# Kernel optimization log

Hardware: AMD Instinct MI355X
Metric: run time of the kernel (lower is better)

The kernel has to match this reference:

```python
import jax, jax.numpy as jnp
import numpy as np

NUM_EXPERTS = 16
TOP_K = 2
HIDDEN = 2048
INTER = 1408
TOKENS = 4096


def setup_inputs() -> dict:
    key = jax.random.key(0)
    k0, k1, k2, k3, k4 = jax.random.split(key, 5)
    scale = 0.02
    return {
        "hidden_states": jax.random.normal(k0, (TOKENS, HIDDEN), jnp.float32),
        "router_logits": jax.random.normal(k1, (TOKENS, NUM_EXPERTS), jnp.float32),
        # SwiGLU expert weights, stacked over the expert dim.
        "w_gate": jax.random.normal(k2, (NUM_EXPERTS, HIDDEN, INTER), jnp.float32) * scale,
        "w_up": jax.random.normal(k3, (NUM_EXPERTS, HIDDEN, INTER), jnp.float32) * scale,
        "w_down": jax.random.normal(k4, (NUM_EXPERTS, INTER, HIDDEN), jnp.float32) * scale,
    }


def reference(hidden_states, router_logits, w_gate, w_up, w_down):
    # Routing (router_use_softmax=False branch): topk on raw logits,
    # then softmax over the selected top-k logits.
    topk_weights, topk_ids = jax.lax.top_k(router_logits, TOP_K)  # [T,K]
    topk_weights = jax.nn.softmax(topk_weights, axis=-1)

    T = hidden_states.shape[0]
    # Dense combine matrix [T, E]: weight of expert e for token t (0 if not selected).
    combine = jnp.zeros((T, NUM_EXPERTS), hidden_states.dtype)
    combine = combine.at[jnp.arange(T)[:, None], topk_ids].add(topk_weights)

    # Expert SwiGLU FFNs, computed densely over all tokens per expert and
    # masked/weighted by the combine matrix (same math as gather->FFN->scatter).
    g = jnp.einsum("th,ehi->eti", hidden_states, w_gate)  # [E,T,I]
    u = jnp.einsum("th,ehi->eti", hidden_states, w_up)    # [E,T,I]
    a = jax.nn.silu(g) * u                                  # [E,T,I]
    y = jnp.einsum("eti,eih->eth", a, w_down)             # [E,T,H]

    # Weighted scatter-combine: sum_e combine[t,e] * y[e,t,:]
    return jnp.einsum("eth,te->th", y, combine)            # [T,H]
```

## Files before the change

### kernel.cpp

```cpp
#include <hip/hip_runtime.h>
#include <hip/hip_bf16.h>
#include <cstdint>

#define NTOK 4096
#define NEXP 16
#define HID 2048
#define INTER 1408
#define BK 32
#define LDA 40
#define MAXTILES 80
#define GU_NB 22
#define DN_NB 32
#define GU_GRID (GU_NB * MAXTILES)
#define DN_GRID (DN_NB * MAXTILES)

typedef __attribute__((ext_vector_type(8))) short bf16x8;
typedef __attribute__((ext_vector_type(4))) float f32x4;


__device__ inline unsigned pack_bf16(float lo, float hi) {
  unsigned a = __builtin_bit_cast(unsigned, lo) + 0x8000u;
  unsigned b = __builtin_bit_cast(unsigned, hi) + 0x8000u;
  return __builtin_amdgcn_perm(b, a, 0x07060302u);
}

__global__ void k_router(const float* __restrict__ logits, int* __restrict__ topk_id,
                         float* __restrict__ topk_w, int* __restrict__ counts) {
  int t = blockIdx.x * blockDim.x + threadIdx.x;
  if (t >= NTOK) return;
  const float* l = logits + (size_t)t * NEXP;
  float b0 = -1e30f, b1 = -1e30f; int i0 = 0, i1 = 0;
#pragma unroll
  for (int i = 0; i < NEXP; i++) {
    float v = l[i];
    if (v > b0) { b1 = b0; i1 = i0; b0 = v; i0 = i; }
    else if (v > b1) { b1 = v; i1 = i; }
  }
  float e = __expf(b1 - b0);
  float inv = 1.f / (1.f + e);
  topk_id[t * 2] = i0; topk_id[t * 2 + 1] = i1;
  topk_w[t * 2] = inv; topk_w[t * 2 + 1] = e * inv;
  atomicAdd(&counts[i0], 1);
  atomicAdd(&counts[i1], 1);
}

__global__ void k_build(int* __restrict__ ws_i) {
  if (threadIdx.x == 0) {
    int off = 0, nt = 0;
    for (int e = 0; e < NEXP; e++) {
      int c = ws_i[e];
      ws_i[32 + e] = off;
      int tiles = (c + 127) >> 7;
      for (int mt = 0; mt < tiles; mt++) { ws_i[64 + nt] = e; ws_i[144 + nt] = mt; nt++; }
      off += c;
    }
    ws_i[48] = nt;
  }
}

__global__ void k_scatter(const int* __restrict__ topk_id, const float* __restrict__ topk_w,
                          int* __restrict__ ws_i, int* __restrict__ list_tok,
                          float* __restrict__ list_w, int* __restrict__ slot_of) {
  int t = blockIdx.x * blockDim.x + threadIdx.x;
  if (t >= NTOK) return;
#pragma unroll
  for (int k = 0; k < 2; k++) {
    int e = topk_id[t * 2 + k];
    int slot = ws_i[32 + e] + atomicAdd(&ws_i[16 + e], 1);
    list_tok[slot] = t;
    list_w[slot] = topk_w[t * 2 + k];
    slot_of[t * 2 + k] = slot;
  }
}

__global__ __launch_bounds__(256) void k_gather(const float* __restrict__ hidden,
                                                const int* __restrict__ list_tok,
                                                unsigned short* __restrict__ Ab) {
  int s = blockIdx.x, tx = threadIdx.x;
  int t = list_tok[s];
  const float4* src = (const float4*)(hidden + (size_t)t * HID) + tx * 2;
  float4 a = src[0], b = src[1];
  uint4 w = make_uint4(pack_bf16(a.x, a.y), pack_bf16(a.z, a.w),
                       pack_bf16(b.x, b.y), pack_bf16(b.z, b.w));
  ((uint4*)(Ab + (size_t)s * HID))[tx] = w;
}

__global__ __launch_bounds__(256, 4) void k_gateup(
    const unsigned short* __restrict__ Ab, const float* __restrict__ w_gate,
    const float* __restrict__ w_up, const int* __restrict__ ws_i,
    __hip_bfloat16* __restrict__ act) {
  __shared__ unsigned short sA[128 * LDA];
  __shared__ unsigned short sBg[64 * LDA];
  __shared__ unsigned short sBu[64 * LDA];

  int bid = blockIdx.x;
  int w = (bid & 7) * (GU_GRID / 8) + (bid >> 3);
  int tileId = w / GU_NB;
  int n0 = (w - tileId * GU_NB) * 64;
  if (tileId >= ws_i[48]) return;
  int e = ws_i[64 + tileId];
  int mt = ws_i[144 + tileId];
  int c = ws_i[e];
  int offE = ws_i[32 + e];
  int m0 = mt * 128;
  int tid = threadIdx.x;

  int lane = tid & 63;
  int wave = tid >> 6;
  int wm = wave & 1, wn = wave >> 1;

  int ar = tid >> 1;
  int ah = (tid & 1) * 16;
  int rA = m0 + ar; int rrA = rA < c ? rA : c - 1;
  const unsigned short* aSrc = Ab + (size_t)(offE + rrA) * HID + ah;

  int bn = tid & 63;
  int bkg = tid >> 6;
  const float* bgSrc = w_gate + (size_t)e * HID * INTER + n0 + bn + (size_t)(bkg * 8) * INTER;
  const float* buSrc = w_up   + (size_t)e * HID * INTER + n0 + bn + (size_t)(bkg * 8) * INTER;

  f32x4 accG[4][2], accU[4][2];
#pragma unroll
  for (int i = 0; i < 4; i++)
#pragma unroll
    for (int j = 0; j < 2; j++) { accG[i][j] = (f32x4)(0.f); accU[i][j] = (f32x4)(0.f); }

  int kq = (lane >> 4) * 8;
  int ml = lane & 15;

  uint4 a0r, a1r; float g[8], u[8];
  {
    const uint4* ap = (const uint4*)aSrc;
    a0r = ap[0]; a1r = ap[1];
#pragma unroll
    for (int j = 0; j < 8; j++) { g[j] = bgSrc[(size_t)j * INTER]; u[j] = buSrc[(size_t)j * INTER]; }
  }

  for (int k0 = 0; k0 < HID; k0 += BK) {
    __syncthreads();
    *(uint4*)&sA[ar * LDA + ah] = a0r;
    *(uint4*)&sA[ar * LDA + ah + 8] = a1r;
    *(uint4*)&sBg[bn * LDA + bkg * 8] = make_uint4(
        pack_bf16(g[0], g[1]), pack_bf16(g[2], g[3]),
        pack_bf16(g[4], g[5]), pack_bf16(g[6], g[7]));
    *(uint4*)&sBu[bn * LDA + bkg * 8] = make_uint4(
        pack_bf16(u[0], u[1]), pack_bf16(u[2], u[3]),
        pack_bf16(u[4], u[5]), pack_bf16(u[6], u[7]));
    __syncthreads();

    if (k0 + BK < HID) {
      const uint4* ap = (const uint4*)(aSrc + k0 + BK);
      a0r = ap[0]; a1r = ap[1];
      const float* bg = bgSrc + (size_t)(k0 + BK) * INTER;
      const float* bu = buSrc + (size_t)(k0 + BK) * INTER;
#pragma unroll
      for (int j = 0; j < 8; j++) { g[j] = bg[(size_t)j * INTER]; u[j] = bu[(size_t)j * INTER]; }
    }

    bf16x8 af[4], bgf[2], buf2[2];
#pragma unroll
    for (int ni = 0; ni < 2; ni++) {
      bgf[ni] = *(const bf16x8*)&sBg[(wn * 32 + ni * 16 + ml) * LDA + kq];
      buf2[ni] = *(const bf16x8*)&sBu[(wn * 32 + ni * 16 + ml) * LDA + kq];
    }
#pragma unroll
    for (int mi = 0; mi < 4; mi++)
      af[mi] = *(const bf16x8*)&sA[(wm * 64 + mi * 16 + ml) * LDA + kq];
#pragma unroll
    for (int mi = 0; mi < 4; mi++)
#pragma unroll
      for (int ni = 0; ni < 2; ni++) {
        accG[mi][ni] = __builtin_amdgcn_mfma_f32_16x16x32_bf16(af[mi], bgf[ni], accG[mi][ni], 0, 0, 0);
        accU[mi][ni] = __builtin_amdgcn_mfma_f32_16x16x32_bf16(af[mi], buf2[ni], accU[mi][ni], 0, 0, 0);
      }
  }

  int rq = (lane >> 4) * 4;
#pragma unroll
  for (int mi = 0; mi < 4; mi++)
#pragma unroll
    for (int r = 0; r < 4; r++) {
      int mrow = wm * 64 + mi * 16 + rq + r;
      int mglob = m0 + mrow;
      if (mglob < c) {
        size_t arow = (size_t)(offE + mglob);
#pragma unroll
        for (int ni = 0; ni < 2; ni++) {
          float gv = accG[mi][ni][r], uv = accU[mi][ni][r];
          float av = gv / (1.f + __expf(-gv)) * uv;
          int ncol = n0 + wn * 32 + ni * 16 + ml;
          act[arow * INTER + ncol] = __float2bfloat16(av);
        }
      }
    }
}

__global__ __launch_bounds__(256, 4) void k_down(
    const __hip_bfloat16* __restrict__ act, const float* __restrict__ w_down,
    const int* __restrict__ ws_i, const float* __restrict__ list_w,
    unsigned short* __restrict__ y) {
  __shared__ unsigned short sA[128 * LDA];
  __shared__ unsigned short sB[64 * LDA];
  __shared__ float sW[128];

  int bid = blockIdx.x;
  int w = (bid & 7) * (DN_GRID / 8) + (bid >> 3);
  int tileId = w >> 5;
  int n0 = (w & 31) * 64;
  if (tileId >= ws_i[48]) return;
  int e = ws_i[64 + tileId];
  int mt = ws_i[144 + tileId];
  int c = ws_i[e];
  int offE = ws_i[32 + e];
  int m0 = mt * 128;
  int tid = threadIdx.x;

  if (tid < 128) {
    int r = m0 + tid;
    int rr = r < c ? r : c - 1;
    sW[tid] = list_w[offE + rr];
  }

  int lane = tid & 63;
  int wave = tid >> 6;
  int wm = wave & 1, wn = wave >> 1;
  f32x4 acc[4][2];
#pragma unroll
  for (int i = 0; i < 4; i++)
#pragma unroll
    for (int j = 0; j < 2; j++) acc[i][j] = (f32x4)(0.f);

  int ar = tid >> 1;
  int ah = (tid & 1) * 16;
  int rA = m0 + ar; int rrA = rA < c ? rA : c - 1;
  const unsigned short* aSrc = (const unsigned short*)act + (size_t)(offE + rrA) * INTER + ah;

  int bn = tid & 63;
  int bkg = tid >> 6;
  const float* bSrc = w_down + (size_t)e * INTER * HID + (size_t)(bkg * 8) * HID + n0 + bn;

  int kq = (lane >> 4) * 8;
  int ml = lane & 15;

  uint4 a0r, a1r; float b[8];
  {
    const uint4* ap = (const uint4*)aSrc;
    a0r = ap[0]; a1r = ap[1];
#pragma unroll
    for (int j = 0; j < 8; j++) b[j] = bSrc[(size_t)j * HID];
  }

  for (int k0 = 0; k0 < INTER; k0 += BK) {
    __syncthreads();
    *(uint4*)&sA[ar * LDA + ah] = a0r;
    *(uint4*)&sA[ar * LDA + ah + 8] = a1r;
    *(uint4*)&sB[bn * LDA + bkg * 8] = make_uint4(
        pack_bf16(b[0], b[1]), pack_bf16(b[2], b[3]),
        pack_bf16(b[4], b[5]), pack_bf16(b[6], b[7]));
    __syncthreads();

    if (k0 + BK < INTER) {
      const uint4* ap = (const uint4*)(aSrc + k0 + BK);
      a0r = ap[0]; a1r = ap[1];
      const float* bp = bSrc + (size_t)(k0 + BK) * HID;
#pragma unroll
      for (int j = 0; j < 8; j++) b[j] = bp[(size_t)j * HID];
    }

    bf16x8 af[4], bf[2];
#pragma unroll
    for (int ni = 0; ni < 2; ni++)
      bf[ni] = *(const bf16x8*)&sB[(wn * 32 + ni * 16 + ml) * LDA + kq];
#pragma unroll
    for (int mi = 0; mi < 4; mi++)
      af[mi] = *(const bf16x8*)&sA[(wm * 64 + mi * 16 + ml) * LDA + kq];
#pragma unroll
    for (int mi = 0; mi < 4; mi++)
#pragma unroll
      for (int ni = 0; ni < 2; ni++)
        acc[mi][ni] = __builtin_amdgcn_mfma_f32_16x16x32_bf16(af[mi], bf[ni], acc[mi][ni], 0, 0, 0);
  }

  int rq = (lane >> 4) * 4;
#pragma unroll
  for (int mi = 0; mi < 4; mi++)
#pragma unroll
    for (int r = 0; r < 4; r++) {
      int mrow = wm * 64 + mi * 16 + rq + r;
      if (m0 + mrow < c) {
        float w2 = sW[mrow];
        size_t yrow = (size_t)(offE + m0 + mrow);
#pragma unroll
        for (int ni = 0; ni < 2; ni++) {
          int ncol = n0 + wn * 32 + ni * 16 + ml;
          float v = w2 * acc[mi][ni][r];
          y[yrow * HID + ncol] = (unsigned short)(pack_bf16(v, 0.f) & 0xffffu);
        }
      }
    }
}

__global__ __launch_bounds__(256) void k_combine(const unsigned short* __restrict__ y,
                                                 const int* __restrict__ slot_of,
                                                 float* __restrict__ out) {
  int t = blockIdx.x, tx = threadIdx.x;
  size_t s0 = (size_t)slot_of[t * 2], s1 = (size_t)slot_of[t * 2 + 1];
  uint4 v0 = ((const uint4*)(y + s0 * HID))[tx];
  uint4 v1 = ((const uint4*)(y + s1 * HID))[tx];
  float r[8];
  unsigned p0[4] = {v0.x, v0.y, v0.z, v0.w};
  unsigned p1[4] = {v1.x, v1.y, v1.z, v1.w};
#pragma unroll
  for (int i = 0; i < 4; i++) {
    float lo0 = __builtin_bit_cast(float, p0[i] << 16);
    float hi0 = __builtin_bit_cast(float, p0[i] & 0xffff0000u);
    float lo1 = __builtin_bit_cast(float, p1[i] << 16);
    float hi1 = __builtin_bit_cast(float, p1[i] & 0xffff0000u);
    r[i * 2] = lo0 + lo1; r[i * 2 + 1] = hi0 + hi1;
  }
  float4* op = (float4*)(out + (size_t)t * HID) + tx * 2;
  op[0] = make_float4(r[0], r[1], r[2], r[3]);
  op[1] = make_float4(r[4], r[5], r[6], r[7]);
}

extern "C" void kernel_launch(void* const* d_in, const int* in_sizes, int n_in,
                              void* d_out, int out_size, void* d_ws, size_t ws_size,
                              hipStream_t stream) {
  const float* hidden = (const float*)d_in[0];
  const float* logits = (const float*)d_in[1];
  const float* w_gate = (const float*)d_in[2];
  const float* w_up = (const float*)d_in[3];
  const float* w_down = (const float*)d_in[4];
  float* out = (float*)d_out;

  int* ws_i = (int*)d_ws;
  int* topk_id = ws_i + 256;
  float* topk_w = (float*)(ws_i + 8448);
  int* list_tok = ws_i + 16640;
  float* list_w = (float*)(ws_i + 24832);
  int* slot_of = ws_i + 33024;
  __hip_bfloat16* act = (__hip_bfloat16*)((char*)d_ws + 262144);
  unsigned short* AbY = (unsigned short*)((char*)d_ws + 23330816);

  hipMemsetAsync(d_ws, 0, 256 * 4, stream);

  k_router<<<NTOK / 256, 256, 0, stream>>>(logits, topk_id, topk_w, ws_i);
  k_build<<<1, 64, 0, stream>>>(ws_i);
  k_scatter<<<NTOK / 256, 256, 0, stream>>>(topk_id, topk_w, ws_i, list_tok, list_w, slot_of);
  k_gather<<<NTOK * 2, 256, 0, stream>>>(hidden, list_tok, AbY);
  k_gateup<<<GU_GRID, 256, 0, stream>>>(AbY, w_gate, w_up, ws_i, act);
  k_down<<<DN_GRID, 256, 0, stream>>>(act, w_down, ws_i, list_w, AbY);
  k_combine<<<NTOK, 256, 0, stream>>>(AbY, slot_of, out);
}
```

Measured before the change: 899.9 us.

## Pre-transpose weights to bf16 and stream tiles via global_load_lds

Adds a transpose-and-convert kernel that writes all expert weights as bf16 in K-contiguous layout into workspace on every call. New gate/up and down GEMM kernels then copy A and B tiles straight into LDS with 16-byte global_load_lds instead of strided fp32 loads packed through registers. The down kernel also widens its N tile to 128. The conversion pass reads and writes every weight (about 277MB of bf16 output) each call, and the direct-to-LDS path drops register prefetch and LDS padding, which may add bank conflicts and load latency. The old path is kept as a fallback when the workspace is too small.

```diff
diff --git a/kernel.cpp b/kernel.cpp
--- a/kernel.cpp
+++ b/kernel.cpp
@@ -11,17 +11,31 @@
 #define MAXTILES 80
 #define GU_NB 22
 #define DN_NB 32
+#define DN_NB2 16
 #define GU_GRID (GU_NB * MAXTILES)
 #define DN_GRID (DN_NB * MAXTILES)
+#define DN_GRID2 (DN_NB2 * MAXTILES)
+
+#define WGT_OFF 56885248ull
+#define WUT_OFF (WGT_OFF + 92274688ull)
+#define WDT_OFF (WUT_OFF + 92274688ull)
+#define WS_NEED (WDT_OFF + 92274688ull)
 
 typedef __attribute__((ext_vector_type(8))) short bf16x8;
 typedef __attribute__((ext_vector_type(4))) float f32x4;
-
 
 __device__ inline unsigned pack_bf16(float lo, float hi) {
   unsigned a = __builtin_bit_cast(unsigned, lo) + 0x8000u;
   unsigned b = __builtin_bit_cast(unsigned, hi) + 0x8000u;
   return __builtin_amdgcn_perm(b, a, 0x07060302u);
+}
+
+typedef __attribute__((address_space(3))) void lds_vt;
+typedef __attribute__((address_space(1))) const void glob_vt;
+__device__ __forceinline__ void gload16(const void* g, void* l) {
+  __builtin_amdgcn_global_load_lds(
+      (glob_vt*)(unsigned long long)g,
+      (lds_vt*)(unsigned)(unsigned long long)l, 16, 0, 0);
 }
 
 __global__ void k_router(const float* __restrict__ logits, int* __restrict__ topk_id,
@@ -85,13 +99,45 @@
   ((uint4*)(Ab + (size_t)s * HID))[tx] = w;
 }
 
-__global__ __launch_bounds__(256, 4) void k_gateup(
-    const unsigned short* __restrict__ Ab, const float* __restrict__ w_gate,
-    const float* __restrict__ w_up, const int* __restrict__ ws_i,
+__global__ __launch_bounds__(256) void k_tconv(const float* __restrict__ src,
+                                               unsigned short* __restrict__ dst,
+                                               int R, int C) {
+  __shared__ unsigned short t[64][68];
+  int e = blockIdx.z, rb = blockIdx.y << 6, cb = blockIdx.x << 6;
+  int tid = threadIdx.x;
+  int lr = tid >> 2, q = tid & 3;
+  const float* sp = src + (size_t)e * R * C + (size_t)(rb + lr) * C + cb + q * 16;
+  float4 v0 = ((const float4*)sp)[0];
+  float4 v1 = ((const float4*)sp)[1];
+  float4 v2 = ((const float4*)sp)[2];
+  float4 v3 = ((const float4*)sp)[3];
+  unsigned* tp = (unsigned*)&t[lr][q * 16];
+  tp[0] = pack_bf16(v0.x, v0.y); tp[1] = pack_bf16(v0.z, v0.w);
+  tp[2] = pack_bf16(v1.x, v1.y); tp[3] = pack_bf16(v1.z, v1.w);
+  tp[4] = pack_bf16(v2.x, v2.y); tp[5] = pack_bf16(v2.z, v2.w);
+  tp[6] = pack_bf16(v3.x, v3.y); tp[7] = pack_bf16(v3.z, v3.w);
+  __syncthreads();
+  int oc = tid >> 2, seg = tid & 3;
+  unsigned o[8];
+#pragma unroll
+  for (int i = 0; i < 8; i++) {
+    unsigned lo = t[seg * 16 + 2 * i][oc];
+    unsigned hi = t[seg * 16 + 2 * i + 1][oc];
+    o[i] = lo | (hi << 16);
+  }
+  unsigned short* dp = dst + (size_t)e * R * C + (size_t)(cb + oc) * R + rb + seg * 16;
+  ((uint4*)dp)[0] = make_uint4(o[0], o[1], o[2], o[3]);
+  ((uint4*)dp)[1] = make_uint4(o[4], o[5], o[6], o[7]);
+}
+
+
+__global__ __launch_bounds__(256, 3) void k_gateup_gl(
+    const unsigned short* __restrict__ Ab, const unsigned short* __restrict__ wgT,
+    const unsigned short* __restrict__ wuT, const int* __restrict__ ws_i,
     __hip_bfloat16* __restrict__ act) {
-  __shared__ unsigned short sA[128 * LDA];
-  __shared__ unsigned short sBg[64 * LDA];
-  __shared__ unsigned short sBu[64 * LDA];
+  __shared__ unsigned short sA[128 * BK];
+  __shared__ unsigned short sBg[64 * BK];
+  __shared__ unsigned short sBu[64 * BK];
 
   int bid = blockIdx.x;
   int w = (bid & 7) * (GU_GRID / 8) + (bid >> 3);
@@ -104,16 +150,209 @@
   int offE = ws_i[32 + e];
   int m0 = mt * 128;
   int tid = threadIdx.x;
-
   int lane = tid & 63;
   int wave = tid >> 6;
   int wm = wave & 1, wn = wave >> 1;
 
+  int la = lane >> 2;
+  int h = (lane & 3) * 16;
+  int rA0 = (wave * 2 + 0) * 16 + la;
+  int rA1 = (wave * 2 + 1) * 16 + la;
+  int gr0 = m0 + rA0; gr0 = gr0 < c ? gr0 : c - 1;
+  int gr1 = m0 + rA1; gr1 = gr1 < c ? gr1 : c - 1;
+  const char* aBase0 = (const char*)(Ab + (size_t)(offE + gr0) * HID) + h;
+  const char* aBase1 = (const char*)(Ab + (size_t)(offE + gr1) * HID) + h;
+  char* ldsA0 = (char*)sA + (wave * 2 + 0) * 1024;
+  char* ldsA1 = (char*)sA + (wave * 2 + 1) * 1024;
+
+  int nB = wave * 16 + la;
+  const char* bgBase = (const char*)(wgT + ((size_t)e * INTER + n0 + nB) * HID) + h;
+  const char* buBase = (const char*)(wuT + ((size_t)e * INTER + n0 + nB) * HID) + h;
+  char* ldsBg = (char*)sBg + wave * 1024;
+  char* ldsBu = (char*)sBu + wave * 1024;
+
+  f32x4 accG[4][2], accU[4][2];
+#pragma unroll
+  for (int i = 0; i < 4; i++)
+#pragma unroll
+    for (int j = 0; j < 2; j++) { accG[i][j] = (f32x4)(0.f); accU[i][j] = (f32x4)(0.f); }
+
+  int kq = (lane >> 4) * 8;
+  int ml = lane & 15;
+
+  for (int k0 = 0; k0 < HID; k0 += BK) {
+    __syncthreads();
+    size_t kb = (size_t)k0 * 2;
+    gload16(aBase0 + kb, ldsA0);
+    gload16(aBase1 + kb, ldsA1);
+    gload16(bgBase + kb, ldsBg);
+    gload16(buBase + kb, ldsBu);
+    __syncthreads();
+
+    bf16x8 af[4], bgf[2], buf2[2];
+#pragma unroll
+    for (int ni = 0; ni < 2; ni++) {
+      bgf[ni] = *(const bf16x8*)&sBg[(wn * 32 + ni * 16 + ml) * BK + kq];
+      buf2[ni] = *(const bf16x8*)&sBu[(wn * 32 + ni * 16 + ml) * BK + kq];
+    }
+#pragma unroll
+    for (int mi = 0; mi < 4; mi++)
+      af[mi] = *(const bf16x8*)&sA[(wm * 64 + mi * 16 + ml) * BK + kq];
+#pragma unroll
+    for (int mi = 0; mi < 4; mi++)
+#pragma unroll
+      for (int ni = 0; ni < 2; ni++) {
+        accG[mi][ni] = __builtin_amdgcn_mfma_f32_16x16x32_bf16(af[mi], bgf[ni], accG[mi][ni], 0, 0, 0);
+        accU[mi][ni] = __builtin_amdgcn_mfma_f32_16x16x32_bf16(af[mi], buf2[ni], accU[mi][ni], 0, 0, 0);
+      }
+  }
+
+  int rq = (lane >> 4) * 4;
+#pragma unroll
+  for (int mi = 0; mi < 4; mi++)
+#pragma unroll
+    for (int r = 0; r < 4; r++) {
+      int mrow = wm * 64 + mi * 16 + rq + r;
+      int mglob = m0 + mrow;
+      if (mglob < c) {
+        size_t arow = (size_t)(offE + mglob);
+#pragma unroll
+        for (int ni = 0; ni < 2; ni++) {
+          float gv = accG[mi][ni][r], uv = accU[mi][ni][r];
+          float av = gv / (1.f + __expf(-gv)) * uv;
+          int ncol = n0 + wn * 32 + ni * 16 + ml;
+          act[arow * INTER + ncol] = __float2bfloat16(av);
+        }
+      }
+    }
+}
+
+__global__ __launch_bounds__(256, 3) void k_down_gl(
+    const unsigned short* __restrict__ act, const unsigned short* __restrict__ wdT,
+    const int* __restrict__ ws_i, const float* __restrict__ list_w,
+    unsigned short* __restrict__ y) {
+  __shared__ unsigned short sA[128 * BK];
+  __shared__ unsigned short sB[128 * BK];
+  __shared__ float sW[128];
+
+  int bid = blockIdx.x;
+  int w = (bid & 7) * (DN_GRID2 / 8) + (bid >> 3);
+  int tileId = w >> 4;
+  int n0 = (w & 15) * 128;
+  if (tileId >= ws_i[48]) return;
+  int e = ws_i[64 + tileId];
+  int mt = ws_i[144 + tileId];
+  int c = ws_i[e];
+  int offE = ws_i[32 + e];
+  int m0 = mt * 128;
+  int tid = threadIdx.x;
+
+  if (tid < 128) {
+    int r = m0 + tid;
+    int rr = r < c ? r : c - 1;
+    sW[tid] = list_w[offE + rr];
+  }
+
+  int lane = tid & 63;
+  int wave = tid >> 6;
+  int wm = wave & 1, wn = wave >> 1;
+
+  int la = lane >> 2;
+  int h = (lane & 3) * 16;
+  int rA0 = (wave * 2 + 0) * 16 + la;
+  int rA1 = (wave * 2 + 1) * 16 + la;
+  int gr0 = m0 + rA0; gr0 = gr0 < c ? gr0 : c - 1;
+  int gr1 = m0 + rA1; gr1 = gr1 < c ? gr1 : c - 1;
+  const char* aBase0 = (const char*)(act + (size_t)(offE + gr0) * INTER) + h;
+  const char* aBase1 = (const char*)(act + (size_t)(offE + gr1) * INTER) + h;
+  char* ldsA0 = (char*)sA + (wave * 2 + 0) * 1024;
+  char* ldsA1 = (char*)sA + (wave * 2 + 1) * 1024;
+
+  int rB0 = (wave * 2 + 0) * 16 + la;
+  int rB1 = (wave * 2 + 1) * 16 + la;
+  const char* bBase0 = (const char*)(wdT + ((size_t)e * HID + n0 + rB0) * INTER) + h;
+  const char* bBase1 = (const char*)(wdT + ((size_t)e * HID + n0 + rB1) * INTER) + h;
+  char* ldsB0 = (char*)sB + (wave * 2 + 0) * 1024;
+  char* ldsB1 = (char*)sB + (wave * 2 + 1) * 1024;
+
+  f32x4 acc[4][4];
+#pragma unroll
+  for (int i = 0; i < 4; i++)
+#pragma unroll
+    for (int j = 0; j < 4; j++) acc[i][j] = (f32x4)(0.f);
+
+  int kq = (lane >> 4) * 8;
+  int ml = lane & 15;
+
+  for (int k0 = 0; k0 < INTER; k0 += BK) {
+    __syncthreads();
+    size_t kb = (size_t)k0 * 2;
+    gload16(aBase0 + kb, ldsA0);
+    gload16(aBase1 + kb, ldsA1);
+    gload16(bBase0 + kb, ldsB0);
+    gload16(bBase1 + kb, ldsB1);
+    __syncthreads();
+
+    bf16x8 af[4], bf[4];
+#pragma unroll
+    for (int ni = 0; ni < 4; ni++)
+      bf[ni] = *(const bf16x8*)&sB[(wn * 64 + ni * 16 + ml) * BK + kq];
+#pragma unroll
+    for (int mi = 0; mi < 4; mi++)
+      af[mi] = *(const bf16x8*)&sA[(wm * 64 + mi * 16 + ml) * BK + kq];
+#pragma unroll
+    for (int mi = 0; mi < 4; mi++)
+#pragma unroll
+      for (int ni = 0; ni < 4; ni++)
+        acc[mi][ni] = __builtin_amdgcn_mfma_f32_16x16x32_bf16(af[mi], bf[ni], acc[mi][ni], 0, 0, 0);
+  }
+
+  int rq = (lane >> 4) * 4;
+#pragma unroll
+  for (int mi = 0; mi < 4; mi++)
+#pragma unroll
+    for (int r = 0; r < 4; r++) {
+      int mrow = wm * 64 + mi * 16 + rq + r;
+      if (m0 + mrow < c) {
+        float w2 = sW[mrow];
+        size_t yrow = (size_t)(offE + m0 + mrow);
+#pragma unroll
+        for (int ni = 0; ni < 4; ni++) {
+          int ncol = n0 + wn * 64 + ni * 16 + ml;
+          float v = w2 * acc[mi][ni][r];
+          y[yrow * HID + ncol] = (unsigned short)(pack_bf16(v, 0.f) & 0xffffu);
+        }
+      }
+    }
+}
+
+
+__global__ __launch_bounds__(256, 4) void k_gateup_rs(
+    const unsigned short* __restrict__ Ab, const float* __restrict__ w_gate,
+    const float* __restrict__ w_up, const int* __restrict__ ws_i,
+    __hip_bfloat16* __restrict__ act) {
+  __shared__ unsigned short sA[128 * LDA];
+  __shared__ unsigned short sBg[64 * LDA];
+  __shared__ unsigned short sBu[64 * LDA];
+
+  int bid = blockIdx.x;
+  int w = (bid & 7) * (GU_GRID / 8) + (bid >> 3);
+  int tileId = w / GU_NB;
+  int n0 = (w - tileId * GU_NB) * 64;
+  if (tileId >= ws_i[48]) return;
+  int e = ws_i[64 + tileId];
+  int mt = ws_i[144 + tileId];
+  int c = ws_i[e];
+  int offE = ws_i[32 + e];
+  int m0 = mt * 128;
+  int tid = threadIdx.x;
+  int lane = tid & 63;
+  int wave = tid >> 6;
+  int wm = wave & 1, wn = wave >> 1;
   int ar = tid >> 1;
   int ah = (tid & 1) * 16;
   int rA = m0 + ar; int rrA = rA < c ? rA : c - 1;
   const unsigned short* aSrc = Ab + (size_t)(offE + rrA) * HID + ah;
-
   int bn = tid & 63;
   int bkg = tid >> 6;
   const float* bgSrc = w_gate + (size_t)e * HID * INTER + n0 + bn + (size_t)(bkg * 8) * INTER;
@@ -124,10 +363,8 @@
   for (int i = 0; i < 4; i++)
 #pragma unroll
     for (int j = 0; j < 2; j++) { accG[i][j] = (f32x4)(0.f); accU[i][j] = (f32x4)(0.f); }
-
   int kq = (lane >> 4) * 8;
   int ml = lane & 15;
-
   uint4 a0r, a1r; float g[8], u[8];
   {
     const uint4* ap = (const uint4*)aSrc;
@@ -135,7 +372,6 @@
 #pragma unroll
     for (int j = 0; j < 8; j++) { g[j] = bgSrc[(size_t)j * INTER]; u[j] = buSrc[(size_t)j * INTER]; }
   }
-
   for (int k0 = 0; k0 < HID; k0 += BK) {
     __syncthreads();
     *(uint4*)&sA[ar * LDA + ah] = a0r;
@@ -147,7 +383,6 @@
         pack_bf16(u[0], u[1]), pack_bf16(u[2], u[3]),
         pack_bf16(u[4], u[5]), pack_bf16(u[6], u[7]));
     __syncthreads();
-
     if (k0 + BK < HID) {
       const uint4* ap = (const uint4*)(aSrc + k0 + BK);
       a0r = ap[0]; a1r = ap[1];
@@ -156,7 +391,6 @@
 #pragma unroll
       for (int j = 0; j < 8; j++) { g[j] = bg[(size_t)j * INTER]; u[j] = bu[(size_t)j * INTER]; }
     }
-
     bf16x8 af[4], bgf[2], buf2[2];
 #pragma unroll
     for (int ni = 0; ni < 2; ni++) {
@@ -174,7 +408,6 @@
         accU[mi][ni] = __builtin_amdgcn_mfma_f32_16x16x32_bf16(af[mi], buf2[ni], accU[mi][ni], 0, 0, 0);
       }
   }
-
   int rq = (lane >> 4) * 4;
 #pragma unroll
   for (int mi = 0; mi < 4; mi++)
@@ -195,14 +428,13 @@
     }
 }
 
-__global__ __launch_bounds__(256, 4) void k_down(
+__global__ __launch_bounds__(256, 4) void k_down_rs(
     const __hip_bfloat16* __restrict__ act, const float* __restrict__ w_down,
     const int* __restrict__ ws_i, const float* __restrict__ list_w,
     unsigned short* __restrict__ y) {
   __shared__ unsigned short sA[128 * LDA];
   __shared__ unsigned short sB[64 * LDA];
   __shared__ float sW[128];
-
   int bid = blockIdx.x;
   int w = (bid & 7) * (DN_GRID / 8) + (bid >> 3);
   int tileId = w >> 5;
@@ -214,13 +446,11 @@
   int offE = ws_i[32 + e];
   int m0 = mt * 128;
   int tid = threadIdx.x;
-
   if (tid < 128) {
     int r = m0 + tid;
     int rr = r < c ? r : c - 1;
     sW[tid] = list_w[offE + rr];
   }
-
   int lane = tid & 63;
   int wave = tid >> 6;
   int wm = wave & 1, wn = wave >> 1;
@@ -229,19 +459,15 @@
   for (int i = 0; i < 4; i++)
 #pragma unroll
     for (int j = 0; j < 2; j++) acc[i][j] = (f32x4)(0.f);
-
   int ar = tid >> 1;
   int ah = (tid & 1) * 16;
   int rA = m0 + ar; int rrA = rA < c ? rA : c - 1;
   const unsigned short* aSrc = (const unsigned short*)act + (size_t)(offE + rrA) * INTER + ah;
-
   int bn = tid & 63;
   int bkg = tid >> 6;
   const float* bSrc = w_down + (size_t)e * INTER * HID + (size_t)(bkg * 8) * HID + n0 + bn;
-
   int kq = (lane >> 4) * 8;
   int ml = lane & 15;
-
   uint4 a0r, a1r; float b[8];
   {
     const uint4* ap = (const uint4*)aSrc;
@@ -249,7 +475,6 @@
 #pragma unroll
     for (int j = 0; j < 8; j++) b[j] = bSrc[(size_t)j * HID];
   }
-
   for (int k0 = 0; k0 < INTER; k0 += BK) {
     __syncthreads();
     *(uint4*)&sA[ar * LDA + ah] = a0r;
@@ -258,7 +483,6 @@
         pack_bf16(b[0], b[1]), pack_bf16(b[2], b[3]),
         pack_bf16(b[4], b[5]), pack_bf16(b[6], b[7]));
     __syncthreads();
-
     if (k0 + BK < INTER) {
       const uint4* ap = (const uint4*)(aSrc + k0 + BK);
       a0r = ap[0]; a1r = ap[1];
@@ -266,7 +490,6 @@
 #pragma unroll
       for (int j = 0; j < 8; j++) b[j] = bp[(size_t)j * HID];
     }
-
     bf16x8 af[4], bf[2];
 #pragma unroll
     for (int ni = 0; ni < 2; ni++)
@@ -280,7 +503,6 @@
       for (int ni = 0; ni < 2; ni++)
         acc[mi][ni] = __builtin_amdgcn_mfma_f32_16x16x32_bf16(af[mi], bf[ni], acc[mi][ni], 0, 0, 0);
   }
-
   int rq = (lane >> 4) * 4;
 #pragma unroll
   for (int mi = 0; mi < 4; mi++)
@@ -348,7 +570,19 @@
   k_build<<<1, 64, 0, stream>>>(ws_i);
   k_scatter<<<NTOK / 256, 256, 0, stream>>>(topk_id, topk_w, ws_i, list_tok, list_w, slot_of);
   k_gather<<<NTOK * 2, 256, 0, stream>>>(hidden, list_tok, AbY);
-  k_gateup<<<GU_GRID, 256, 0, stream>>>(AbY, w_gate, w_up, ws_i, act);
-  k_down<<<DN_GRID, 256, 0, stream>>>(act, w_down, ws_i, list_w, AbY);
+
+  if (ws_size >= WS_NEED) {
+    unsigned short* wgT = (unsigned short*)((char*)d_ws + WGT_OFF);
+    unsigned short* wuT = (unsigned short*)((char*)d_ws + WUT_OFF);
+    unsigned short* wdT = (unsigned short*)((char*)d_ws + WDT_OFF);
+    k_tconv<<<dim3(INTER / 64, HID / 64, NEXP), 256, 0, stream>>>(w_gate, wgT, HID, INTER);
+    k_tconv<<<dim3(INTER / 64, HID / 64, NEXP), 256, 0, stream>>>(w_up, wuT, HID, INTER);
+    k_tconv<<<dim3(HID / 64, INTER / 64, NEXP), 256, 0, stream>>>(w_down, wdT, INTER, HID);
+    k_gateup_gl<<<GU_GRID, 256, 0, stream>>>(AbY, wgT, wuT, ws_i, act);
+    k_down_gl<<<DN_GRID2, 256, 0, stream>>>((const unsigned short*)act, wdT, ws_i, list_w, AbY);
+  } else {
+    k_gateup_rs<<<GU_GRID, 256, 0, stream>>>(AbY, w_gate, w_up, ws_i, act);
+    k_down_rs<<<DN_GRID, 256, 0, stream>>>(act, w_down, ws_i, list_w, AbY);
+  }
   k_combine<<<NTOK, 256, 0, stream>>>(AbY, slot_of, out);
 }
```

Result: faster. 854.2 us (-5.1%).

## Load GEMM tiles directly to LDS via global_load_lds, widen down-proj N tile

Applied to the files above, without the earlier changes.

Both expert GEMM kernels now stage A and fp32 weight tiles straight from global memory into LDS with the global_load_lds builtin, replacing the register-staged prefetch and convert-on-store path. The fp32 weights are kept in LDS and converted to bf16 at fragment-read time. The down-projection tile grows from 64 to 128 columns, halving its grid, and occupancy hints drop from 4 to 3. This removes the register software pipelining (there is no double buffering now), so load latency is exposed between barriers, and the column-strided fp32 LDS reads may cause bank conflicts.

```diff
diff --git a/kernel.cpp b/kernel.cpp
--- a/kernel.cpp
+++ b/kernel.cpp
@@ -7,10 +7,9 @@
 #define HID 2048
 #define INTER 1408
 #define BK 32
-#define LDA 40
 #define MAXTILES 80
 #define GU_NB 22
-#define DN_NB 32
+#define DN_NB 16
 #define GU_GRID (GU_NB * MAXTILES)
 #define DN_GRID (DN_NB * MAXTILES)
 
@@ -22,6 +21,14 @@
   unsigned a = __builtin_bit_cast(unsigned, lo) + 0x8000u;
   unsigned b = __builtin_bit_cast(unsigned, hi) + 0x8000u;
   return __builtin_amdgcn_perm(b, a, 0x07060302u);
+}
+
+typedef __attribute__((address_space(3))) void lds_vt;
+typedef __attribute__((address_space(1))) const void glob_vt;
+__device__ __forceinline__ void gload16(const void* g, void* l) {
+  __builtin_amdgcn_global_load_lds(
+      (glob_vt*)(unsigned long long)g,
+      (lds_vt*)(unsigned)(unsigned long long)l, 16, 0, 0);
 }
 
 __global__ void k_router(const float* __restrict__ logits, int* __restrict__ topk_id,
@@ -85,13 +92,13 @@
   ((uint4*)(Ab + (size_t)s * HID))[tx] = w;
 }
 
-__global__ __launch_bounds__(256, 4) void k_gateup(
+__global__ __launch_bounds__(256, 3) void k_gateup_f(
     const unsigned short* __restrict__ Ab, const float* __restrict__ w_gate,
     const float* __restrict__ w_up, const int* __restrict__ ws_i,
     __hip_bfloat16* __restrict__ act) {
-  __shared__ unsigned short sA[128 * LDA];
-  __shared__ unsigned short sBg[64 * LDA];
-  __shared__ unsigned short sBu[64 * LDA];
+  __shared__ unsigned short sA[128 * BK];
+  __shared__ float sG[BK * 64];
+  __shared__ float sU[BK * 64];
 
   int bid = blockIdx.x;
   int w = (bid & 7) * (GU_GRID / 8) + (bid >> 3);
@@ -104,20 +111,31 @@
   int offE = ws_i[32 + e];
   int m0 = mt * 128;
   int tid = threadIdx.x;
-
   int lane = tid & 63;
   int wave = tid >> 6;
   int wm = wave & 1, wn = wave >> 1;
 
-  int ar = tid >> 1;
-  int ah = (tid & 1) * 16;
-  int rA = m0 + ar; int rrA = rA < c ? rA : c - 1;
-  const unsigned short* aSrc = Ab + (size_t)(offE + rrA) * HID + ah;
-
-  int bn = tid & 63;
-  int bkg = tid >> 6;
-  const float* bgSrc = w_gate + (size_t)e * HID * INTER + n0 + bn + (size_t)(bkg * 8) * INTER;
-  const float* buSrc = w_up   + (size_t)e * HID * INTER + n0 + bn + (size_t)(bkg * 8) * INTER;
+  int la = lane >> 2;
+  int h = (lane & 3) * 16;
+  int gr0 = m0 + wave * 32 + la;      gr0 = gr0 < c ? gr0 : c - 1;
+  int gr1 = m0 + wave * 32 + 16 + la; gr1 = gr1 < c ? gr1 : c - 1;
+  const char* aBase0 = (const char*)(Ab + (size_t)(offE + gr0) * HID) + h;
+  const char* aBase1 = (const char*)(Ab + (size_t)(offE + gr1) * HID) + h;
+  char* ldsA0 = (char*)sA + (wave * 2 + 0) * 1024;
+  char* ldsA1 = (char*)sA + (wave * 2 + 1) * 1024;
+
+  int kr = lane >> 4;
+  int hb = (lane & 15) * 16;
+  int kB0 = wave * 8 + kr;
+  int kB1 = wave * 8 + 4 + kr;
+  const char* gBase0 = (const char*)(w_gate + (size_t)e * HID * INTER + (size_t)kB0 * INTER + n0) + hb;
+  const char* gBase1 = (const char*)(w_gate + (size_t)e * HID * INTER + (size_t)kB1 * INTER + n0) + hb;
+  const char* uBase0 = (const char*)(w_up   + (size_t)e * HID * INTER + (size_t)kB0 * INTER + n0) + hb;
+  const char* uBase1 = (const char*)(w_up   + (size_t)e * HID * INTER + (size_t)kB1 * INTER + n0) + hb;
+  char* ldsG0 = (char*)sG + (wave * 2 + 0) * 1024;
+  char* ldsG1 = (char*)sG + (wave * 2 + 1) * 1024;
+  char* ldsU0 = (char*)sU + (wave * 2 + 0) * 1024;
+  char* ldsU1 = (char*)sU + (wave * 2 + 1) * 1024;
 
   f32x4 accG[4][2], accU[4][2];
 #pragma unroll
@@ -127,45 +145,40 @@
 
   int kq = (lane >> 4) * 8;
   int ml = lane & 15;
-
-  uint4 a0r, a1r; float g[8], u[8];
-  {
-    const uint4* ap = (const uint4*)aSrc;
-    a0r = ap[0]; a1r = ap[1];
-#pragma unroll
-    for (int j = 0; j < 8; j++) { g[j] = bgSrc[(size_t)j * INTER]; u[j] = buSrc[(size_t)j * INTER]; }
-  }
+  int nB0 = wn * 32 + ml;
 
   for (int k0 = 0; k0 < HID; k0 += BK) {
     __syncthreads();
-    *(uint4*)&sA[ar * LDA + ah] = a0r;
-    *(uint4*)&sA[ar * LDA + ah + 8] = a1r;
-    *(uint4*)&sBg[bn * LDA + bkg * 8] = make_uint4(
-        pack_bf16(g[0], g[1]), pack_bf16(g[2], g[3]),
-        pack_bf16(g[4], g[5]), pack_bf16(g[6], g[7]));
-    *(uint4*)&sBu[bn * LDA + bkg * 8] = make_uint4(
-        pack_bf16(u[0], u[1]), pack_bf16(u[2], u[3]),
-        pack_bf16(u[4], u[5]), pack_bf16(u[6], u[7]));
+    size_t ab = (size_t)k0 * 2;
+    size_t bb = (size_t)k0 * INTER * 4;
+    gload16(aBase0 + ab, ldsA0);
+    gload16(aBase1 + ab, ldsA1);
+    gload16(gBase0 + bb, ldsG0);
+    gload16(gBase1 + bb, ldsG1);
+    gload16(uBase0 + bb, ldsU0);
+    gload16(uBase1 + bb, ldsU1);
     __syncthreads();
 
-    if (k0 + BK < HID) {
-      const uint4* ap = (const uint4*)(aSrc + k0 + BK);
-      a0r = ap[0]; a1r = ap[1];
-      const float* bg = bgSrc + (size_t)(k0 + BK) * INTER;
-      const float* bu = buSrc + (size_t)(k0 + BK) * INTER;
-#pragma unroll
-      for (int j = 0; j < 8; j++) { g[j] = bg[(size_t)j * INTER]; u[j] = bu[(size_t)j * INTER]; }
-    }
-
     bf16x8 af[4], bgf[2], buf2[2];
 #pragma unroll
+    for (int mi = 0; mi < 4; mi++)
+      af[mi] = *(const bf16x8*)&sA[(wm * 64 + mi * 16 + ml) * BK + kq];
+#pragma unroll
     for (int ni = 0; ni < 2; ni++) {
-      bgf[ni] = *(const bf16x8*)&sBg[(wn * 32 + ni * 16 + ml) * LDA + kq];
-      buf2[ni] = *(const bf16x8*)&sBu[(wn * 32 + ni * 16 + ml) * LDA + kq];
-    }
-#pragma unroll
-    for (int mi = 0; mi < 4; mi++)
-      af[mi] = *(const bf16x8*)&sA[(wm * 64 + mi * 16 + ml) * LDA + kq];
+      int nb = nB0 + ni * 16;
+      float tg[8], tu[8];
+#pragma unroll
+      for (int i = 0; i < 8; i++) {
+        tg[i] = sG[(kq + i) * 64 + nb];
+        tu[i] = sU[(kq + i) * 64 + nb];
+      }
+      union { uint4 q; bf16x8 v; } cg, cu;
+      cg.q = make_uint4(pack_bf16(tg[0], tg[1]), pack_bf16(tg[2], tg[3]),
+                        pack_bf16(tg[4], tg[5]), pack_bf16(tg[6], tg[7]));
+      cu.q = make_uint4(pack_bf16(tu[0], tu[1]), pack_bf16(tu[2], tu[3]),
+                        pack_bf16(tu[4], tu[5]), pack_bf16(tu[6], tu[7]));
+      bgf[ni] = cg.v; buf2[ni] = cu.v;
+    }
 #pragma unroll
     for (int mi = 0; mi < 4; mi++)
 #pragma unroll
@@ -195,18 +208,18 @@
     }
 }
 
-__global__ __launch_bounds__(256, 4) void k_down(
-    const __hip_bfloat16* __restrict__ act, const float* __restrict__ w_down,
+__global__ __launch_bounds__(256, 3) void k_down_f(
+    const unsigned short* __restrict__ act, const float* __restrict__ w_down,
     const int* __restrict__ ws_i, const float* __restrict__ list_w,
     unsigned short* __restrict__ y) {
-  __shared__ unsigned short sA[128 * LDA];
-  __shared__ unsigned short sB[64 * LDA];
+  __shared__ unsigned short sA[128 * BK];
+  __shared__ float sB[BK * 128];
   __shared__ float sW[128];
 
   int bid = blockIdx.x;
   int w = (bid & 7) * (DN_GRID / 8) + (bid >> 3);
-  int tileId = w >> 5;
-  int n0 = (w & 31) * 64;
+  int tileId = w >> 4;
+  int n0 = (w & 15) * 128;
   if (tileId >= ws_i[48]) return;
   int e = ws_i[64 + tileId];
   int mt = ws_i[144 + tileId];
@@ -224,60 +237,62 @@
   int lane = tid & 63;
   int wave = tid >> 6;
   int wm = wave & 1, wn = wave >> 1;
-  f32x4 acc[4][2];
+
+  int la = lane >> 2;
+  int h = (lane & 3) * 16;
+  int gr0 = m0 + wave * 32 + la;      gr0 = gr0 < c ? gr0 : c - 1;
+  int gr1 = m0 + wave * 32 + 16 + la; gr1 = gr1 < c ? gr1 : c - 1;
+  const char* aBase0 = (const char*)(act + (size_t)(offE + gr0) * INTER) + h;
+  const char* aBase1 = (const char*)(act + (size_t)(offE + gr1) * INTER) + h;
+  char* ldsA0 = (char*)sA + (wave * 2 + 0) * 1024;
+  char* ldsA1 = (char*)sA + (wave * 2 + 1) * 1024;
+
+  int krd = lane >> 5;
+  int hd = (lane & 31) * 16;
+  const char* bRoot = (const char*)(w_down + (size_t)e * INTER * HID + n0);
+  char* ldsBw = (char*)sB + wave * 4096;
+
+  f32x4 acc[4][4];
 #pragma unroll
   for (int i = 0; i < 4; i++)
 #pragma unroll
-    for (int j = 0; j < 2; j++) acc[i][j] = (f32x4)(0.f);
-
-  int ar = tid >> 1;
-  int ah = (tid & 1) * 16;
-  int rA = m0 + ar; int rrA = rA < c ? rA : c - 1;
-  const unsigned short* aSrc = (const unsigned short*)act + (size_t)(offE + rrA) * INTER + ah;
-
-  int bn = tid & 63;
-  int bkg = tid >> 6;
-  const float* bSrc = w_down + (size_t)e * INTER * HID + (size_t)(bkg * 8) * HID + n0 + bn;
+    for (int j = 0; j < 4; j++) acc[i][j] = (f32x4)(0.f);
 
   int kq = (lane >> 4) * 8;
   int ml = lane & 15;
-
-  uint4 a0r, a1r; float b[8];
-  {
-    const uint4* ap = (const uint4*)aSrc;
-    a0r = ap[0]; a1r = ap[1];
-#pragma unroll
-    for (int j = 0; j < 8; j++) b[j] = bSrc[(size_t)j * HID];
-  }
+  int nB0 = wn * 64 + ml;
 
   for (int k0 = 0; k0 < INTER; k0 += BK) {
     __syncthreads();
-    *(uint4*)&sA[ar * LDA + ah] = a0r;
-    *(uint4*)&sA[ar * LDA + ah + 8] = a1r;
-    *(uint4*)&sB[bn * LDA + bkg * 8] = make_uint4(
-        pack_bf16(b[0], b[1]), pack_bf16(b[2], b[3]),
-        pack_bf16(b[4], b[5]), pack_bf16(b[6], b[7]));
+    size_t ab = (size_t)k0 * 2;
+    gload16(aBase0 + ab, ldsA0);
+    gload16(aBase1 + ab, ldsA1);
+#pragma unroll
+    for (int cch = 0; cch < 4; cch++) {
+      size_t kk = (size_t)(k0 + wave * 8 + cch * 2 + krd);
+      gload16(bRoot + kk * HID * 4 + hd, ldsBw + cch * 1024);
+    }
     __syncthreads();
 
-    if (k0 + BK < INTER) {
-      const uint4* ap = (const uint4*)(aSrc + k0 + BK);
-      a0r = ap[0]; a1r = ap[1];
-      const float* bp = bSrc + (size_t)(k0 + BK) * HID;
-#pragma unroll
-      for (int j = 0; j < 8; j++) b[j] = bp[(size_t)j * HID];
-    }
-
-    bf16x8 af[4], bf[2];
-#pragma unroll
-    for (int ni = 0; ni < 2; ni++)
-      bf[ni] = *(const bf16x8*)&sB[(wn * 32 + ni * 16 + ml) * LDA + kq];
+    bf16x8 af[4], bf[4];
 #pragma unroll
     for (int mi = 0; mi < 4; mi++)
-      af[mi] = *(const bf16x8*)&sA[(wm * 64 + mi * 16 + ml) * LDA + kq];
+      af[mi] = *(const bf16x8*)&sA[(wm * 64 + mi * 16 + ml) * BK + kq];
+#pragma unroll
+    for (int ni = 0; ni < 4; ni++) {
+      int nb = nB0 + ni * 16;
+      float t[8];
+#pragma unroll
+      for (int i = 0; i < 8; i++) t[i] = sB[(kq + i) * 128 + nb];
+      union { uint4 q; bf16x8 v; } cb;
+      cb.q = make_uint4(pack_bf16(t[0], t[1]), pack_bf16(t[2], t[3]),
+                        pack_bf16(t[4], t[5]), pack_bf16(t[6], t[7]));
+      bf[ni] = cb.v;
+    }
 #pragma unroll
     for (int mi = 0; mi < 4; mi++)
 #pragma unroll
-      for (int ni = 0; ni < 2; ni++)
+      for (int ni = 0; ni < 4; ni++)
         acc[mi][ni] = __builtin_amdgcn_mfma_f32_16x16x32_bf16(af[mi], bf[ni], acc[mi][ni], 0, 0, 0);
   }
 
@@ -291,8 +306,8 @@
         float w2 = sW[mrow];
         size_t yrow = (size_t)(offE + m0 + mrow);
 #pragma unroll
-        for (int ni = 0; ni < 2; ni++) {
-          int ncol = n0 + wn * 32 + ni * 16 + ml;
+        for (int ni = 0; ni < 4; ni++) {
+          int ncol = n0 + wn * 64 + ni * 16 + ml;
           float v = w2 * acc[mi][ni][r];
           y[yrow * HID + ncol] = (unsigned short)(pack_bf16(v, 0.f) & 0xffffu);
         }
@@ -348,7 +363,7 @@
   k_build<<<1, 64, 0, stream>>>(ws_i);
   k_scatter<<<NTOK / 256, 256, 0, stream>>>(topk_id, topk_w, ws_i, list_tok, list_w, slot_of);
   k_gather<<<NTOK * 2, 256, 0, stream>>>(hidden, list_tok, AbY);
-  k_gateup<<<GU_GRID, 256, 0, stream>>>(AbY, w_gate, w_up, ws_i, act);
-  k_down<<<DN_GRID, 256, 0, stream>>>(act, w_down, ws_i, list_w, AbY);
+  k_gateup_f<<<GU_GRID, 256, 0, stream>>>(AbY, w_gate, w_up, ws_i, act);
+  k_down_f<<<DN_GRID, 256, 0, stream>>>((const unsigned short*)act, w_down, ws_i, list_w, AbY);
   k_combine<<<NTOK, 256, 0, stream>>>(AbY, slot_of, out);
 }
```

After: 833.6 us. 7.4% less time.
